# Kernel tuning notes

Hardware: AMD Instinct MI355X
Metric: run time of the kernel (lower is better)

## Reference

```python
import jax, jax.numpy as jnp
import numpy as np

BS = 8  # DCT block size


def _dct_basis():
    x = np.arange(BS)
    u = np.arange(BS)
    M = 0.5 * np.cos((2 * x[None, :] + 1) * u[:, None] * np.pi / 16)
    M[0, :] *= 1.0 / np.sqrt(2.0)
    # Separable 2-D basis: coeff[u, v, x, y] = M[u, x] * M[v, y]
    return jnp.asarray(np.einsum('ux,vy->uvxy', M, M), jnp.float32)


_Q_LUM = np.array([
    [16, 11, 10, 16, 24, 40, 51, 61],
    [12, 12, 14, 19, 26, 58, 60, 55],
    [14, 13, 16, 24, 40, 57, 69, 56],
    [14, 17, 22, 29, 51, 87, 80, 62],
    [18, 22, 37, 56, 68, 109, 103, 77],
    [24, 35, 55, 64, 81, 104, 113, 92],
    [49, 64, 78, 87, 103, 121, 120, 101],
    [72, 92, 95, 98, 112, 100, 103, 99]], dtype=np.float32)

_Q_CHROM = np.array([
    [17, 18, 24, 47, 99, 99, 99, 99],
    [18, 21, 26, 66, 99, 99, 99, 99],
    [24, 26, 56, 99, 99, 99, 99, 99],
    [47, 66, 99, 99, 99, 99, 99, 99],
    [99, 99, 99, 99, 99, 99, 99, 99],
    [99, 99, 99, 99, 99, 99, 99, 99],
    [99, 99, 99, 99, 99, 99, 99, 99],
    [99, 99, 99, 99, 99, 99, 99, 99]], dtype=np.float32)


def setup_inputs() -> dict:
    key = jax.random.key(0)
    image = jax.random.uniform(key, (16, 3, 512, 512), dtype=jnp.float32)
    rgb2yuv = jnp.array([[0.299, 0.587, 0.114],
                         [-0.1687, -0.3313, 0.5],
                         [0.5, -0.4187, -0.0813]], jnp.float32)
    yuv2rgb = jnp.array([[1.0, 0.0, 1.402],
                         [1.0, -0.34414, -0.71414],
                         [1.0, 1.772, 0.0]], jnp.float32)
    return {
        'image': image,
        'rgb2yuv': rgb2yuv,
        'yuv2rgb': yuv2rgb,
        'dct_coeff': _dct_basis(),          # (8,8,8,8)
        'q_lum': jnp.asarray(_Q_LUM),       # (8,8)
        'q_chrom': jnp.asarray(_Q_CHROM),   # (8,8)
    }


def _compress(x, C, Q):
    # x: (b, c, H, W) with H, W multiples of 8; C: (8,8,8,8); Q: (8,8)
    b, c, H, W = x.shape
    nh, nw = H // BS, W // BS
    x = x * 255.0 - 128.0
    # tile into 8x8 blocks: (b, c, nh, nw, 8, 8)
    blk = x.reshape(b, c, nh, BS, nw, BS).transpose(0, 1, 2, 4, 3, 5)
    # forward block DCT: out[u,v] = sum_{x,y} C[u,v,x,y] * blk[x,y]
    d = jnp.einsum('uvxy,bcnmxy->bcnmuv', C, blk)
    # quantize / dequantize (Q broadcasts over the last two (u, v) dims)
    d = jnp.round(d / Q) * Q
    # inverse block DCT (transpose of the orthonormal basis)
    r = jnp.einsum('xyuv,bcnmuv->bcnmxy', C, d)
    img = r.transpose(0, 1, 2, 4, 3, 5).reshape(b, c, H, W)
    return (img + 128.0) / 255.0


def reference(image, rgb2yuv, yuv2rgb, dct_coeff, q_lum, q_chrom):
    yuv = jnp.einsum('ij,bjhw->bihw', rgb2yuv, image)
    y = _compress(yuv[:, 0:1], dct_coeff, q_lum)
    uv = _compress(yuv[:, 1:], dct_coeff, q_chrom)
    out = jnp.einsum('ij,bjhw->bihw', yuv2rgb, jnp.concatenate([y, uv], axis=1))
    return out
```

## Files before the change

kernel.cpp:

```cpp
#include <hip/hip_runtime.h>
#include <math.h>

#define CSTRIDE (512 * 512)

typedef float v2f __attribute__((ext_vector_type(2)));

__device__ __forceinline__ float chain_dot64_nofma(const float* __restrict__ c,
                                                   const float* __restrict__ v)
{
#pragma clang fp contract(off)
    float s = 0.0f;
#pragma unroll
    for (int q = 0; q < 64; ++q) s = s + c[q] * v[q];
    return s;
}

__global__ void init_pc(const float* __restrict__ dctC, v2f* __restrict__ pc)
{
    const int idx = blockIdx.x * 256 + threadIdx.x;
    const int jp = idx >> 6, q = idx & 63;
    const int w = jp >> 3, j = jp & 7;
    v2f c;
    c.x = dctC[(size_t)(16 * w + j) * 64 + q];
    c.y = dctC[(size_t)(16 * w + j + 8) * 64 + q];
    pc[idx] = c;
}

__global__ __launch_bounds__(256, 3)
void jpeg_kernel_pk(const float* __restrict__ img,
                    const float* __restrict__ rgb2yuv,
                    const float* __restrict__ yuv2rgb,
                    const float* __restrict__ dctC,
                    const float* __restrict__ qlum,
                    const float* __restrict__ qchrom,
                    float* __restrict__ out,
                    const v2f* __restrict__ pc)
{
#pragma clang fp contract(off)
    __shared__ float V[3][4096];

    const int tid  = threadIdx.x;
    const int lane = tid & 63;
    const int wv   = tid >> 6;
    const int p0u  = __builtin_amdgcn_readfirstlane(wv * 16);
    const int jb   = __builtin_amdgcn_readfirstlane(wv * 8);

    const int b  = blockIdx.x >> 6;
    const int y0 = (blockIdx.x & 63) << 3;
    const size_t base0 = (size_t)b * 3 * CSTRIDE + (size_t)y0 * 512;

    const float r00 = rgb2yuv[0], r01 = rgb2yuv[1], r02 = rgb2yuv[2];
    const float r10 = rgb2yuv[3], r11 = rgb2yuv[4], r12 = rgb2yuv[5];
    const float r20 = rgb2yuv[6], r21 = rgb2yuv[7], r22 = rgb2yuv[8];

#pragma unroll
    for (int i = 0; i < 4; ++i) {
        const size_t f4 = 4 * (size_t)(tid + 256 * i);
        const float4 R4 = *(const float4*)(img + base0 + f4);
        const float4 G4 = *(const float4*)(img + base0 + CSTRIDE + f4);
        const float4 B4 = *(const float4*)(img + base0 + 2 * CSTRIDE + f4);
        const float* rp = (const float*)&R4;
        const float* gp = (const float*)&G4;
        const float* bp = (const float*)&B4;
#pragma unroll
        for (int jj = 0; jj < 4; ++jj) {
            const int flat = 4 * (tid + 256 * i) + jj;
            const int w = flat & 511, x = flat >> 9;
            const int idx = ((x << 3) + (w & 7)) * 64 + (w >> 3);
            const float r_ = rp[jj], g_ = gp[jj], b_ = bp[jj];
            float t;
            t = (r00 * r_ + r01 * g_) + r02 * b_;  V[0][idx] = t * 255.0f - 128.0f;
            t = (r10 * r_ + r11 * g_) + r12 * b_;  V[1][idx] = t * 255.0f - 128.0f;
            t = (r20 * r_ + r21 * g_) + r22 * b_;  V[2][idx] = t * 255.0f - 128.0f;
        }
    }
    __syncthreads();

    const int xb = __builtin_amdgcn_readfirstlane(wv * 2);
    float mrow[2][8];
#pragma unroll
    for (int k = 0; k < 2; ++k)
#pragma unroll
        for (int u = 0; u < 8; ++u)
            mrow[k][u] = dctC[(size_t)(xb + k) * 512 + u * 8] * 2.82842712474619f;

    const float MT[8][8] = {
        { 0.353553391f,  0.353553391f,  0.353553391f,  0.353553391f,  0.353553391f,  0.353553391f,  0.353553391f,  0.353553391f},
        { 0.490392640f,  0.415734806f,  0.277785117f,  0.097545161f, -0.097545161f, -0.277785117f, -0.415734806f, -0.490392640f},
        { 0.461939766f,  0.191341716f, -0.191341716f, -0.461939766f, -0.461939766f, -0.191341716f,  0.191341716f,  0.461939766f},
        { 0.415734806f, -0.097545161f, -0.490392640f, -0.277785117f,  0.277785117f,  0.490392640f,  0.097545161f, -0.415734806f},
        { 0.353553391f, -0.353553391f, -0.353553391f,  0.353553391f,  0.353553391f, -0.353553391f, -0.353553391f,  0.353553391f},
        { 0.277785117f, -0.490392640f,  0.097545161f,  0.415734806f, -0.415734806f, -0.097545161f,  0.490392640f, -0.277785117f},
        { 0.191341716f, -0.461939766f,  0.461939766f, -0.191341716f, -0.191341716f,  0.461939766f, -0.461939766f,  0.191341716f},
        { 0.097545161f, -0.277785117f,  0.415734806f, -0.490392640f,  0.490392640f, -0.415734806f,  0.277785117f, -0.097545161f}};

    for (int c = 0; c < 3; ++c) {
        float* Vc = V[c];

        v2f v2[32];
#pragma unroll
        for (int qq = 0; qq < 32; ++qq) {
            v2f t;
            t.x = Vc[(2 * qq) * 64 + lane];
            t.y = Vc[(2 * qq + 1) * 64 + lane];
            v2[qq] = t;
        }
        __syncthreads();

        const float* qtab = (c == 0) ? qlum : qchrom;
        for (int j = 0; j < 8; ++j) {
            const v2f* crow = pc + (size_t)(jb + j) * 64;
            v2f acc; acc.x = 0.0f; acc.y = 0.0f;
#pragma unroll
            for (int q = 0; q < 64; ++q) {
                const v2f c2 = crow[q];
                v2f p2;
                if ((q & 1) == 0)
                    asm("v_pk_mul_f32 %0, %1, %2 op_sel:[0,0] op_sel_hi:[1,0]"
                        : "=v"(p2) : "s"(c2), "v"(v2[q >> 1]));
                else
                    asm("v_pk_mul_f32 %0, %1, %2 op_sel:[0,1] op_sel_hi:[1,1]"
                        : "=v"(p2) : "s"(c2), "v"(v2[q >> 1]));
                asm("v_pk_add_f32 %0, %0, %1 op_sel:[0,0] op_sel_hi:[1,1]"
                    : "+v"(acc) : "v"(p2));
            }
            const float qA = qtab[p0u + j];
            const float qB = qtab[p0u + j + 8];
            const float dqA = rintf(acc.x / qA) * qA;
            const float dqB = rintf(acc.y / qB) * qB;
            Vc[(p0u + j) * 64 + lane]     = dqA;
            Vc[(p0u + j + 8) * 64 + lane] = dqB;
        }
        __syncthreads();

        float t[64];
#pragma unroll
        for (int u = 0; u < 8; ++u) {
            float du[8];
#pragma unroll
            for (int q = 0; q < 8; ++q) du[q] = Vc[(u * 8 + q) * 64 + lane];
#pragma unroll
            for (int y = 0; y < 8; ++y) {
                float s = MT[y][0] * du[0];
#pragma unroll
                for (int q = 1; q < 8; ++q) s = fmaf(MT[y][q], du[q], s);
                t[u * 8 + y] = s;
            }
        }
        __syncthreads();

#pragma unroll
        for (int j = 0; j < 16; ++j) {
            const int k = j >> 3, y = j & 7;
            float s = mrow[k][0] * t[y];
#pragma unroll
            for (int u = 1; u < 8; ++u) s = fmaf(mrow[k][u], t[u * 8 + y], s);
            Vc[(p0u + j) * 64 + lane] = s;
        }
    }
    __syncthreads();

    const float s255 = 1.0f / 255.0f;
    const float c00 = yuv2rgb[0] * s255, c01 = yuv2rgb[1] * s255, c02 = yuv2rgb[2] * s255;
    const float c10 = yuv2rgb[3] * s255, c11 = yuv2rgb[4] * s255, c12 = yuv2rgb[5] * s255;
    const float c20 = yuv2rgb[6] * s255, c21 = yuv2rgb[7] * s255, c22 = yuv2rgb[8] * s255;
    const float k0 = (yuv2rgb[0] + yuv2rgb[1] + yuv2rgb[2]) * (128.0f / 255.0f);
    const float k1 = (yuv2rgb[3] + yuv2rgb[4] + yuv2rgb[5]) * (128.0f / 255.0f);
    const float k2 = (yuv2rgb[6] + yuv2rgb[7] + yuv2rgb[8]) * (128.0f / 255.0f);

#pragma unroll
    for (int i = 0; i < 4; ++i) {
        float4 o0, o1, o2;
        float* q0 = (float*)&o0; float* q1 = (float*)&o1; float* q2 = (float*)&o2;
#pragma unroll
        for (int jj = 0; jj < 4; ++jj) {
            const int flat = 4 * (tid + 256 * i) + jj;
            const int w = flat & 511, x = flat >> 9;
            const int cell = ((x << 3) + (w & 7)) * 64 + (w >> 3);
            const float Yv = V[0][cell], Uv = V[1][cell], Wv = V[2][cell];
            q0[jj] = fmaf(c00, Yv, fmaf(c01, Uv, fmaf(c02, Wv, k0)));
            q1[jj] = fmaf(c10, Yv, fmaf(c11, Uv, fmaf(c12, Wv, k1)));
            q2[jj] = fmaf(c20, Yv, fmaf(c21, Uv, fmaf(c22, Wv, k2)));
        }
        const size_t f4 = 4 * (size_t)(tid + 256 * i);
        *(float4*)(out + base0 + f4)                = o0;
        *(float4*)(out + base0 + CSTRIDE + f4)      = o1;
        *(float4*)(out + base0 + 2 * CSTRIDE + f4)  = o2;
    }
}

__global__ __launch_bounds__(256, 3)
void jpeg_kernel_sc(const float* __restrict__ img,
                    const float* __restrict__ rgb2yuv,
                    const float* __restrict__ yuv2rgb,
                    const float* __restrict__ dctC,
                    const float* __restrict__ qlum,
                    const float* __restrict__ qchrom,
                    float* __restrict__ out)
{
#pragma clang fp contract(off)
    __shared__ float V[3][4096];

    const int tid  = threadIdx.x;
    const int lane = tid & 63;
    const int wv   = tid >> 6;
    const int p0u  = __builtin_amdgcn_readfirstlane(wv * 16);

    const int b  = blockIdx.x >> 6;
    const int y0 = (blockIdx.x & 63) << 3;
    const size_t base0 = (size_t)b * 3 * CSTRIDE + (size_t)y0 * 512;

    const float r00 = rgb2yuv[0], r01 = rgb2yuv[1], r02 = rgb2yuv[2];
    const float r10 = rgb2yuv[3], r11 = rgb2yuv[4], r12 = rgb2yuv[5];
    const float r20 = rgb2yuv[6], r21 = rgb2yuv[7], r22 = rgb2yuv[8];

#pragma unroll
    for (int i = 0; i < 4; ++i) {
        const size_t f4 = 4 * (size_t)(tid + 256 * i);
        const float4 R4 = *(const float4*)(img + base0 + f4);
        const float4 G4 = *(const float4*)(img + base0 + CSTRIDE + f4);
        const float4 B4 = *(const float4*)(img + base0 + 2 * CSTRIDE + f4);
        const float* rp = (const float*)&R4;
        const float* gp = (const float*)&G4;
        const float* bp = (const float*)&B4;
#pragma unroll
        for (int jj = 0; jj < 4; ++jj) {
            const int flat = 4 * (tid + 256 * i) + jj;
            const int w = flat & 511, x = flat >> 9;
            const int idx = ((x << 3) + (w & 7)) * 64 + (w >> 3);
            const float r_ = rp[jj], g_ = gp[jj], b_ = bp[jj];
            float t;
            t = (r00 * r_ + r01 * g_) + r02 * b_;  V[0][idx] = t * 255.0f - 128.0f;
            t = (r10 * r_ + r11 * g_) + r12 * b_;  V[1][idx] = t * 255.0f - 128.0f;
            t = (r20 * r_ + r21 * g_) + r22 * b_;  V[2][idx] = t * 255.0f - 128.0f;
        }
    }
    __syncthreads();

    const int xb = __builtin_amdgcn_readfirstlane(wv * 2);
    float mrow[2][8];
#pragma unroll
    for (int k = 0; k < 2; ++k)
#pragma unroll
        for (int u = 0; u < 8; ++u)
            mrow[k][u] = dctC[(size_t)(xb + k) * 512 + u * 8] * 2.82842712474619f;

    const float MT[8][8] = {
        { 0.353553391f,  0.353553391f,  0.353553391f,  0.353553391f,  0.353553391f,  0.353553391f,  0.353553391f,  0.353553391f},
        { 0.490392640f,  0.415734806f,  0.277785117f,  0.097545161f, -0.097545161f, -0.277785117f, -0.415734806f, -0.490392640f},
        { 0.461939766f,  0.191341716f, -0.191341716f, -0.461939766f, -0.461939766f, -0.191341716f,  0.191341716f,  0.461939766f},
        { 0.415734806f, -0.097545161f, -0.490392640f, -0.277785117f,  0.277785117f,  0.490392640f,  0.097545161f, -0.415734806f},
        { 0.353553391f, -0.353553391f, -0.353553391f,  0.353553391f,  0.353553391f, -0.353553391f, -0.353553391f,  0.353553391f},
        { 0.277785117f, -0.490392640f,  0.097545161f,  0.415734806f, -0.415734806f, -0.097545161f,  0.490392640f, -0.277785117f},
        { 0.191341716f, -0.461939766f,  0.461939766f, -0.191341716f, -0.191341716f,  0.461939766f, -0.461939766f,  0.191341716f},
        { 0.097545161f, -0.277785117f,  0.415734806f, -0.490392640f,  0.490392640f, -0.415734806f,  0.277785117f, -0.097545161f}};

    for (int c = 0; c < 3; ++c) {
        float* Vc = V[c];
        float v[64];
#pragma unroll
        for (int q = 0; q < 64; ++q) v[q] = Vc[q * 64 + lane];
        __syncthreads();

        const float* qtab = (c == 0) ? qlum : qchrom;
        for (int j = 0; j < 16; ++j) {
            const float* Crow = dctC + (size_t)(p0u + j) * 64;
            const float d  = chain_dot64_nofma(Crow, v);
            const float qv = qtab[p0u + j];
            const float dq = rintf(d / qv) * qv;
            Vc[(p0u + j) * 64 + lane] = dq;
        }
        __syncthreads();

        float t[64];
#pragma unroll
        for (int u = 0; u < 8; ++u) {
            float du[8];
#pragma unroll
            for (int q = 0; q < 8; ++q) du[q] = Vc[(u * 8 + q) * 64 + lane];
#pragma unroll
            for (int y = 0; y < 8; ++y) {
                float s = MT[y][0] * du[0];
#pragma unroll
                for (int q = 1; q < 8; ++q) s = fmaf(MT[y][q], du[q], s);
                t[u * 8 + y] = s;
            }
        }
        __syncthreads();

#pragma unroll
        for (int j = 0; j < 16; ++j) {
            const int k = j >> 3, y = j & 7;
            float s = mrow[k][0] * t[y];
#pragma unroll
            for (int u = 1; u < 8; ++u) s = fmaf(mrow[k][u], t[u * 8 + y], s);
            Vc[(p0u + j) * 64 + lane] = s;
        }
    }
    __syncthreads();

    const float s255 = 1.0f / 255.0f;
    const float c00 = yuv2rgb[0] * s255, c01 = yuv2rgb[1] * s255, c02 = yuv2rgb[2] * s255;
    const float c10 = yuv2rgb[3] * s255, c11 = yuv2rgb[4] * s255, c12 = yuv2rgb[5] * s255;
    const float c20 = yuv2rgb[6] * s255, c21 = yuv2rgb[7] * s255, c22 = yuv2rgb[8] * s255;
    const float k0 = (yuv2rgb[0] + yuv2rgb[1] + yuv2rgb[2]) * (128.0f / 255.0f);
    const float k1 = (yuv2rgb[3] + yuv2rgb[4] + yuv2rgb[5]) * (128.0f / 255.0f);
    const float k2 = (yuv2rgb[6] + yuv2rgb[7] + yuv2rgb[8]) * (128.0f / 255.0f);

#pragma unroll
    for (int i = 0; i < 4; ++i) {
        float4 o0, o1, o2;
        float* q0 = (float*)&o0; float* q1 = (float*)&o1; float* q2 = (float*)&o2;
#pragma unroll
        for (int jj = 0; jj < 4; ++jj) {
            const int flat = 4 * (tid + 256 * i) + jj;
            const int w = flat & 511, x = flat >> 9;
            const int cell = ((x << 3) + (w & 7)) * 64 + (w >> 3);
            const float Yv = V[0][cell], Uv = V[1][cell], Wv = V[2][cell];
            q0[jj] = fmaf(c00, Yv, fmaf(c01, Uv, fmaf(c02, Wv, k0)));
            q1[jj] = fmaf(c10, Yv, fmaf(c11, Uv, fmaf(c12, Wv, k1)));
            q2[jj] = fmaf(c20, Yv, fmaf(c21, Uv, fmaf(c22, Wv, k2)));
        }
        const size_t f4 = 4 * (size_t)(tid + 256 * i);
        *(float4*)(out + base0 + f4)                = o0;
        *(float4*)(out + base0 + CSTRIDE + f4)      = o1;
        *(float4*)(out + base0 + 2 * CSTRIDE + f4)  = o2;
    }
}

extern "C" void kernel_launch(void* const* d_in, const int* in_sizes, int n_in,
                              void* d_out, int out_size, void* d_ws, size_t ws_size,
                              hipStream_t stream) {
    const float* img = (const float*)d_in[0];
    const float* r2y = (const float*)d_in[1];
    const float* y2r = (const float*)d_in[2];
    const float* C   = (const float*)d_in[3];
    const float* ql  = (const float*)d_in[4];
    const float* qc  = (const float*)d_in[5];
    float* o = (float*)d_out;

    if (ws_size >= 2048 * sizeof(v2f)) {
        v2f* pc = (v2f*)d_ws;
        init_pc<<<dim3(8), dim3(256), 0, stream>>>(C, pc);
        jpeg_kernel_pk<<<dim3(16 * 64), dim3(256), 0, stream>>>(img, r2y, y2r, C, ql, qc, o, pc);
    } else {
        jpeg_kernel_sc<<<dim3(16 * 64), dim3(256), 0, stream>>>(img, r2y, y2r, C, ql, qc, o);
    }
}
```

Before: 168.5 us.

## Replace packed-FP32 DCT with persistent work-stealing kernel using scalar dot

Drops the packed v_pk_mul/v_pk_add forward DCT and its precomputed coefficient-pair table, going back to a scalar 64-term dot product read straight from the DCT basis. The main kernel becomes persistent: a fixed grid of 768 blocks handles the 1024 row tiles and fetches further tile indices through a global atomic counter, which is cleared by a memset before each launch. The aim is to even out tail imbalance across CUs and remove the extra init kernel. In exchange the forward DCT issues more scalar ALU instructions, and each tile adds an atomic plus extra barriers.

```diff
diff --git a/kernel.cpp b/kernel.cpp
--- a/kernel.cpp
+++ b/kernel.cpp
@@ -2,8 +2,8 @@
 #include <math.h>
 
 #define CSTRIDE (512 * 512)
-
-typedef float v2f __attribute__((ext_vector_type(2)));
+#define NTILES  1024
+#define GRID    768
 
 __device__ __forceinline__ float chain_dot64_nofma(const float* __restrict__ c,
                                                    const float* __restrict__ v)
@@ -15,66 +15,28 @@
     return s;
 }
 
-__global__ void init_pc(const float* __restrict__ dctC, v2f* __restrict__ pc)
-{
-    const int idx = blockIdx.x * 256 + threadIdx.x;
-    const int jp = idx >> 6, q = idx & 63;
-    const int w = jp >> 3, j = jp & 7;
-    v2f c;
-    c.x = dctC[(size_t)(16 * w + j) * 64 + q];
-    c.y = dctC[(size_t)(16 * w + j + 8) * 64 + q];
-    pc[idx] = c;
-}
-
 __global__ __launch_bounds__(256, 3)
-void jpeg_kernel_pk(const float* __restrict__ img,
-                    const float* __restrict__ rgb2yuv,
-                    const float* __restrict__ yuv2rgb,
-                    const float* __restrict__ dctC,
-                    const float* __restrict__ qlum,
-                    const float* __restrict__ qchrom,
-                    float* __restrict__ out,
-                    const v2f* __restrict__ pc)
+void jpeg_kernel(const float* __restrict__ img,
+                 const float* __restrict__ rgb2yuv,
+                 const float* __restrict__ yuv2rgb,
+                 const float* __restrict__ dctC,
+                 const float* __restrict__ qlum,
+                 const float* __restrict__ qchrom,
+                 float* __restrict__ out,
+                 unsigned int* __restrict__ counter)
 {
 #pragma clang fp contract(off)
     __shared__ float V[3][4096];
+    __shared__ int nextT;
 
     const int tid  = threadIdx.x;
     const int lane = tid & 63;
     const int wv   = tid >> 6;
     const int p0u  = __builtin_amdgcn_readfirstlane(wv * 16);
-    const int jb   = __builtin_amdgcn_readfirstlane(wv * 8);
-
-    const int b  = blockIdx.x >> 6;
-    const int y0 = (blockIdx.x & 63) << 3;
-    const size_t base0 = (size_t)b * 3 * CSTRIDE + (size_t)y0 * 512;
 
     const float r00 = rgb2yuv[0], r01 = rgb2yuv[1], r02 = rgb2yuv[2];
     const float r10 = rgb2yuv[3], r11 = rgb2yuv[4], r12 = rgb2yuv[5];
     const float r20 = rgb2yuv[6], r21 = rgb2yuv[7], r22 = rgb2yuv[8];
-
-#pragma unroll
-    for (int i = 0; i < 4; ++i) {
-        const size_t f4 = 4 * (size_t)(tid + 256 * i);
-        const float4 R4 = *(const float4*)(img + base0 + f4);
-        const float4 G4 = *(const float4*)(img + base0 + CSTRIDE + f4);
-        const float4 B4 = *(const float4*)(img + base0 + 2 * CSTRIDE + f4);
-        const float* rp = (const float*)&R4;
-        const float* gp = (const float*)&G4;
-        const float* bp = (const float*)&B4;
-#pragma unroll
-        for (int jj = 0; jj < 4; ++jj) {
-            const int flat = 4 * (tid + 256 * i) + jj;
-            const int w = flat & 511, x = flat >> 9;
-            const int idx = ((x << 3) + (w & 7)) * 64 + (w >> 3);
-            const float r_ = rp[jj], g_ = gp[jj], b_ = bp[jj];
-            float t;
-            t = (r00 * r_ + r01 * g_) + r02 * b_;  V[0][idx] = t * 255.0f - 128.0f;
-            t = (r10 * r_ + r11 * g_) + r12 * b_;  V[1][idx] = t * 255.0f - 128.0f;
-            t = (r20 * r_ + r21 * g_) + r22 * b_;  V[2][idx] = t * 255.0f - 128.0f;
-        }
-    }
-    __syncthreads();
 
     const int xb = __builtin_amdgcn_readfirstlane(wv * 2);
     float mrow[2][8];
@@ -94,72 +56,6 @@
         { 0.191341716f, -0.461939766f,  0.461939766f, -0.191341716f, -0.191341716f,  0.461939766f, -0.461939766f,  0.191341716f},
         { 0.097545161f, -0.277785117f,  0.415734806f, -0.490392640f,  0.490392640f, -0.415734806f,  0.277785117f, -0.097545161f}};
 
-    for (int c = 0; c < 3; ++c) {
-        float* Vc = V[c];
-
-        v2f v2[32];
-#pragma unroll
-        for (int qq = 0; qq < 32; ++qq) {
-            v2f t;
-            t.x = Vc[(2 * qq) * 64 + lane];
-            t.y = Vc[(2 * qq + 1) * 64 + lane];
-            v2[qq] = t;
-        }
-        __syncthreads();
-
-        const float* qtab = (c == 0) ? qlum : qchrom;
-        for (int j = 0; j < 8; ++j) {
-            const v2f* crow = pc + (size_t)(jb + j) * 64;
-            v2f acc; acc.x = 0.0f; acc.y = 0.0f;
-#pragma unroll
-            for (int q = 0; q < 64; ++q) {
-                const v2f c2 = crow[q];
-                v2f p2;
-                if ((q & 1) == 0)
-                    asm("v_pk_mul_f32 %0, %1, %2 op_sel:[0,0] op_sel_hi:[1,0]"
-                        : "=v"(p2) : "s"(c2), "v"(v2[q >> 1]));
-                else
-                    asm("v_pk_mul_f32 %0, %1, %2 op_sel:[0,1] op_sel_hi:[1,1]"
-                        : "=v"(p2) : "s"(c2), "v"(v2[q >> 1]));
-                asm("v_pk_add_f32 %0, %0, %1 op_sel:[0,0] op_sel_hi:[1,1]"
-                    : "+v"(acc) : "v"(p2));
-            }
-            const float qA = qtab[p0u + j];
-            const float qB = qtab[p0u + j + 8];
-            const float dqA = rintf(acc.x / qA) * qA;
-            const float dqB = rintf(acc.y / qB) * qB;
-            Vc[(p0u + j) * 64 + lane]     = dqA;
-            Vc[(p0u + j + 8) * 64 + lane] = dqB;
-        }
-        __syncthreads();
-
-        float t[64];
-#pragma unroll
-        for (int u = 0; u < 8; ++u) {
-            float du[8];
-#pragma unroll
-            for (int q = 0; q < 8; ++q) du[q] = Vc[(u * 8 + q) * 64 + lane];
-#pragma unroll
-            for (int y = 0; y < 8; ++y) {
-                float s = MT[y][0] * du[0];
-#pragma unroll
-                for (int q = 1; q < 8; ++q) s = fmaf(MT[y][q], du[q], s);
-                t[u * 8 + y] = s;
-            }
-        }
-        __syncthreads();
-
-#pragma unroll
-        for (int j = 0; j < 16; ++j) {
-            const int k = j >> 3, y = j & 7;
-            float s = mrow[k][0] * t[y];
-#pragma unroll
-            for (int u = 1; u < 8; ++u) s = fmaf(mrow[k][u], t[u * 8 + y], s);
-            Vc[(p0u + j) * 64 + lane] = s;
-        }
-    }
-    __syncthreads();
-
     const float s255 = 1.0f / 255.0f;
     const float c00 = yuv2rgb[0] * s255, c01 = yuv2rgb[1] * s255, c02 = yuv2rgb[2] * s255;
     const float c10 = yuv2rgb[3] * s255, c11 = yuv2rgb[4] * s255, c12 = yuv2rgb[5] * s255;
@@ -168,35 +64,117 @@
     const float k1 = (yuv2rgb[3] + yuv2rgb[4] + yuv2rgb[5]) * (128.0f / 255.0f);
     const float k2 = (yuv2rgb[6] + yuv2rgb[7] + yuv2rgb[8]) * (128.0f / 255.0f);
 
-#pragma unroll
-    for (int i = 0; i < 4; ++i) {
-        float4 o0, o1, o2;
-        float* q0 = (float*)&o0; float* q1 = (float*)&o1; float* q2 = (float*)&o2;
-#pragma unroll
-        for (int jj = 0; jj < 4; ++jj) {
-            const int flat = 4 * (tid + 256 * i) + jj;
-            const int w = flat & 511, x = flat >> 9;
-            const int cell = ((x << 3) + (w & 7)) * 64 + (w >> 3);
-            const float Yv = V[0][cell], Uv = V[1][cell], Wv = V[2][cell];
-            q0[jj] = fmaf(c00, Yv, fmaf(c01, Uv, fmaf(c02, Wv, k0)));
-            q1[jj] = fmaf(c10, Yv, fmaf(c11, Uv, fmaf(c12, Wv, k1)));
-            q2[jj] = fmaf(c20, Yv, fmaf(c21, Uv, fmaf(c22, Wv, k2)));
-        }
-        const size_t f4 = 4 * (size_t)(tid + 256 * i);
-        *(float4*)(out + base0 + f4)                = o0;
-        *(float4*)(out + base0 + CSTRIDE + f4)      = o1;
-        *(float4*)(out + base0 + 2 * CSTRIDE + f4)  = o2;
+    int tile = blockIdx.x;
+
+    while (true) {
+        const int b  = tile >> 6;
+        const int y0 = (tile & 63) << 3;
+        const size_t base0 = (size_t)b * 3 * CSTRIDE + (size_t)y0 * 512;
+
+#pragma unroll
+        for (int i = 0; i < 4; ++i) {
+            const size_t f4 = 4 * (size_t)(tid + 256 * i);
+            const float4 R4 = *(const float4*)(img + base0 + f4);
+            const float4 G4 = *(const float4*)(img + base0 + CSTRIDE + f4);
+            const float4 B4 = *(const float4*)(img + base0 + 2 * CSTRIDE + f4);
+            const float* rp = (const float*)&R4;
+            const float* gp = (const float*)&G4;
+            const float* bp = (const float*)&B4;
+#pragma unroll
+            for (int jj = 0; jj < 4; ++jj) {
+                const int flat = 4 * (tid + 256 * i) + jj;
+                const int w = flat & 511, x = flat >> 9;
+                const int idx = ((x << 3) + (w & 7)) * 64 + (w >> 3);
+                const float r_ = rp[jj], g_ = gp[jj], b_ = bp[jj];
+                float t;
+                t = (r00 * r_ + r01 * g_) + r02 * b_;  V[0][idx] = t * 255.0f - 128.0f;
+                t = (r10 * r_ + r11 * g_) + r12 * b_;  V[1][idx] = t * 255.0f - 128.0f;
+                t = (r20 * r_ + r21 * g_) + r22 * b_;  V[2][idx] = t * 255.0f - 128.0f;
+            }
+        }
+        __syncthreads();
+
+        for (int c = 0; c < 3; ++c) {
+            float* Vc = V[c];
+
+            float v[64];
+#pragma unroll
+            for (int q = 0; q < 64; ++q) v[q] = Vc[q * 64 + lane];
+            __syncthreads();
+
+            const float* qtab = (c == 0) ? qlum : qchrom;
+            for (int j = 0; j < 16; ++j) {
+                const float* Crow = dctC + (size_t)(p0u + j) * 64;
+                const float d  = chain_dot64_nofma(Crow, v);
+                const float qv = qtab[p0u + j];
+                const float dq = rintf(d / qv) * qv;
+                Vc[(p0u + j) * 64 + lane] = dq;
+            }
+            __syncthreads();
+
+            float t[64];
+#pragma unroll
+            for (int u = 0; u < 8; ++u) {
+                float du[8];
+#pragma unroll
+                for (int q = 0; q < 8; ++q) du[q] = Vc[(u * 8 + q) * 64 + lane];
+#pragma unroll
+                for (int y = 0; y < 8; ++y) {
+                    float s = MT[y][0] * du[0];
+#pragma unroll
+                    for (int q = 1; q < 8; ++q) s = fmaf(MT[y][q], du[q], s);
+                    t[u * 8 + y] = s;
+                }
+            }
+            __syncthreads();
+
+#pragma unroll
+            for (int j = 0; j < 16; ++j) {
+                const int k = j >> 3, y = j & 7;
+                float s = mrow[k][0] * t[y];
+#pragma unroll
+                for (int u = 1; u < 8; ++u) s = fmaf(mrow[k][u], t[u * 8 + y], s);
+                Vc[(p0u + j) * 64 + lane] = s;
+            }
+        }
+        __syncthreads();
+
+#pragma unroll
+        for (int i = 0; i < 4; ++i) {
+            float4 o0, o1, o2;
+            float* q0 = (float*)&o0; float* q1 = (float*)&o1; float* q2 = (float*)&o2;
+#pragma unroll
+            for (int jj = 0; jj < 4; ++jj) {
+                const int flat = 4 * (tid + 256 * i) + jj;
+                const int w = flat & 511, x = flat >> 9;
+                const int cell = ((x << 3) + (w & 7)) * 64 + (w >> 3);
+                const float Yv = V[0][cell], Uv = V[1][cell], Wv = V[2][cell];
+                q0[jj] = fmaf(c00, Yv, fmaf(c01, Uv, fmaf(c02, Wv, k0)));
+                q1[jj] = fmaf(c10, Yv, fmaf(c11, Uv, fmaf(c12, Wv, k1)));
+                q2[jj] = fmaf(c20, Yv, fmaf(c21, Uv, fmaf(c22, Wv, k2)));
+            }
+            const size_t f4 = 4 * (size_t)(tid + 256 * i);
+            *(float4*)(out + base0 + f4)                = o0;
+            *(float4*)(out + base0 + CSTRIDE + f4)      = o1;
+            *(float4*)(out + base0 + 2 * CSTRIDE + f4)  = o2;
+        }
+
+        __syncthreads();
+        if (tid == 0) nextT = GRID + (int)atomicAdd(counter, 1u);
+        __syncthreads();
+        tile = nextT;
+        if (tile >= NTILES) break;
     }
 }
 
 __global__ __launch_bounds__(256, 3)
-void jpeg_kernel_sc(const float* __restrict__ img,
-                    const float* __restrict__ rgb2yuv,
-                    const float* __restrict__ yuv2rgb,
-                    const float* __restrict__ dctC,
-                    const float* __restrict__ qlum,
-                    const float* __restrict__ qchrom,
-                    float* __restrict__ out)
+void jpeg_kernel_static(const float* __restrict__ img,
+                        const float* __restrict__ rgb2yuv,
+                        const float* __restrict__ yuv2rgb,
+                        const float* __restrict__ dctC,
+                        const float* __restrict__ qlum,
+                        const float* __restrict__ qchrom,
+                        float* __restrict__ out)
 {
 #pragma clang fp contract(off)
     __shared__ float V[3][4096];
@@ -339,11 +317,11 @@
     const float* qc  = (const float*)d_in[5];
     float* o = (float*)d_out;
 
-    if (ws_size >= 2048 * sizeof(v2f)) {
-        v2f* pc = (v2f*)d_ws;
-        init_pc<<<dim3(8), dim3(256), 0, stream>>>(C, pc);
-        jpeg_kernel_pk<<<dim3(16 * 64), dim3(256), 0, stream>>>(img, r2y, y2r, C, ql, qc, o, pc);
+    if (ws_size >= sizeof(unsigned int)) {
+        unsigned int* cnt = (unsigned int*)d_ws;
+        hipMemsetAsync(cnt, 0, sizeof(unsigned int), stream);
+        jpeg_kernel<<<dim3(GRID), dim3(256), 0, stream>>>(img, r2y, y2r, C, ql, qc, o, cnt);
     } else {
-        jpeg_kernel_sc<<<dim3(16 * 64), dim3(256), 0, stream>>>(img, r2y, y2r, C, ql, qc, o);
+        jpeg_kernel_static<<<dim3(NTILES), dim3(256), 0, stream>>>(img, r2y, y2r, C, ql, qc, o);
     }
 }
```

After: 161.9 us. 3.9% less time.
